# Kernel tuning notes

Hardware: AMD Instinct MI355X
Metric: run time of the kernel (lower is better)

Reference implementation:

```python
import jax, jax.numpy as jnp
import numpy as np

B, N, D = 8, 192, 768   # batch of docs, events per doc, embed_dim
H = 150                 # Score hidden_dim
PAD = -1000.0           # pad_and_stack fill value


def setup_inputs() -> dict:
    key = jax.random.key(0)
    ks = jax.random.split(key, 7)
    s1 = 1.0 / np.sqrt(3 * D)
    s2 = 1.0 / np.sqrt(H)
    return {
        "event_embed": jax.random.normal(ks[0], (B, N, D), jnp.float32),
        "W1": jax.random.normal(ks[1], (3 * D, H), jnp.float32) * s1,
        "b1": jnp.zeros((H,), jnp.float32),
        "W2": jax.random.normal(ks[2], (H, H), jnp.float32) * s2,
        "b2": jnp.zeros((H,), jnp.float32),
        "W3": jax.random.normal(ks[3], (H, 1), jnp.float32) * s2,
        "b3": jnp.zeros((1,), jnp.float32),
    }


def reference(event_embed, W1, b1, W2, b2, W3, b3):
    Bq, Nq, Dq = event_embed.shape
    # antecedent pairs: for each event i, all k < i (row-major, matches torch loop order)
    rows, cols = jnp.tril_indices(Nq, k=-1)          # [P], P = N*(N-1)/2
    i_g = event_embed[:, rows]                        # [B, P, D]
    j_g = event_embed[:, cols]                        # [B, P, D]
    pairs = jnp.concatenate([i_g, j_g, i_g * j_g], axis=-1)  # [B, P, 3D]
    # Score MLP (dropout is identity at inference)
    h = jax.nn.relu(pairs @ W1 + b1)                  # [B, P, H]
    h = jax.nn.relu(h @ W2 + b2)                      # [B, P, H]
    s = (h @ W3 + b3)[..., 0]                         # [B, P]
    # Scatter pair scores into [B, N, N]; diagonal stays 0 = epsilon score.
    logits = jnp.zeros((Bq, Nq, Nq), event_embed.dtype).at[:, rows, cols].set(s)
    tri = jnp.tril(jnp.ones((Nq, Nq), dtype=bool))    # valid cols: k <= i (incl epsilon)
    masked = jnp.where(tri, logits, -jnp.inf)
    probs = jax.nn.softmax(masked, axis=-1)           # ragged softmax per event row
    return jnp.where(tri, probs, jnp.asarray(PAD, probs.dtype))  # pad_and_stack(value=-1000)
```

## Files before the change

### kernel.cpp

```cpp
#include <hip/hip_runtime.h>
#include <hip/hip_bf16.h>

#define NSEQ   192
#define PADV   -1000.0f
#define NEGINF -1.0e30f

typedef __bf16 bf16x8 __attribute__((ext_vector_type(8)));
typedef float  f32x4  __attribute__((ext_vector_type(4)));

__device__ __forceinline__ void glds16(const void* g, void* l) {
  __builtin_amdgcn_global_load_lds(
      (const __attribute__((address_space(1))) unsigned int*)g,
      (__attribute__((address_space(3))) unsigned int*)l, 16, 0, 0);
}

#define MFMA16(a, b, c) __builtin_amdgcn_mfma_f32_16x16x32_bf16((a), (b), (c), 0, 0, 0)

__global__ __launch_bounds__(256) void prep_pack(const float* __restrict__ W1,
                                                 const float* __restrict__ W2,
                                                 __bf16* __restrict__ W1abp,
                                                 __bf16* __restrict__ W1cp,
                                                 __bf16* __restrict__ W2p) {
  int idx = blockIdx.x * 256 + threadIdx.x;
  if (idx < 245760) {
    int e = idx & 7, l = (idx >> 3) & 63, t = idx >> 9;
    int ct = t % 20, kk = t / 20;
    int k = kk * 32 + ((l >> 4) << 3) + e;
    int hp = ct * 16 + (l & 15);
    int col = (hp < 160) ? hp : hp - 160;
    int rbase = (hp < 160) ? 0 : 768;
    float v = (col < 150) ? W1[(size_t)(rbase + k) * 150 + col] : 0.f;
    W1abp[idx] = (__bf16)v;
  } else if (idx < 393216) {
    int j = idx - 245760;
    int kk = j / 6144, rem = j % 6144;
    int q = rem >> 9, l = (rem >> 3) & 63, e = rem & 7;
    int k = kk * 32 + ((l >> 4) << 3) + e;
    int h = q * 16 + (l & 15);
    float v = (q < 10 && h < 150) ? W1[(size_t)(1536 + k) * 150 + h] : 0.f;
    W1cp[j] = (__bf16)v;
  } else {
    int j = idx - 393216;
    int s = j / 6144, rem = j % 6144;
    int q = rem >> 9, l = (rem >> 3) & 63, e = rem & 7;
    int k = s * 32 + ((l >> 4) << 3) + e;
    int h = q * 16 + (l & 15);
    float v = (q < 10 && k < 150 && h < 150) ? W2[(size_t)k * 150 + h] : 0.f;
    W2p[j] = (__bf16)v;
  }
}

__global__ __launch_bounds__(256) void prep_gemm(const float* __restrict__ E,
                                                 const __bf16* __restrict__ W1abp,
                                                 float* __restrict__ A12) {
  int tid = threadIdx.x;
  int w = tid >> 6, l = tid & 63, m = l & 15, kg = l >> 4;
  int mt = blockIdx.x >> 3;
  int c  = blockIdx.x & 7;
  const float* ep = E + (size_t)(mt * 16 + m) * 768 + c * 96;

  f32x4 acc[5];
#pragma unroll
  for (int u = 0; u < 5; ++u) acc[u] = (f32x4){0.f, 0.f, 0.f, 0.f};

#pragma unroll
  for (int kk = 0; kk < 3; ++kk) {
    int k = kk * 32 + kg * 8;
    f32x4 x0 = *(const f32x4*)(ep + k);
    f32x4 x1 = *(const f32x4*)(ep + k + 4);
    bf16x8 af;
#pragma unroll
    for (int e = 0; e < 4; ++e) { af[e] = (__bf16)x0[e]; af[e + 4] = (__bf16)x1[e]; }
    const bf16x8* wp = (const bf16x8*)W1abp + (size_t)(((c * 3 + kk) * 20) + w * 5) * 64 + l;
#pragma unroll
    for (int u = 0; u < 5; ++u)
      acc[u] = MFMA16(af, wp[u * 64], acc[u]);
  }
#pragma unroll
  for (int u = 0; u < 5; ++u)
#pragma unroll
    for (int r = 0; r < 4; ++r)
      atomicAdd(&A12[(size_t)(mt * 16 + kg * 4 + r) * 320 + (w * 5 + u) * 16 + m], acc[u][r]);
}

__global__ __launch_bounds__(256, 2) void pair_mlp(
    const float* __restrict__ E, const float* __restrict__ A12,
    const __bf16* __restrict__ W1cp, const __bf16* __restrict__ W2p,
    const float* __restrict__ b1, const float* __restrict__ b2,
    const float* __restrict__ W3, const float* __restrict__ b3,
    float* __restrict__ out) {
  __shared__ alignas(16) char pool[73728];
  __bf16* Wb  = (__bf16*)pool;
  char*   eib = pool + 24576;
  char*   ejb = pool + 49152;
  char*   h1b = pool + 24576;

  const int tid = threadIdx.x;
  const int w = tid >> 6, l = tid & 63;
  const int m = l & 15, kg = l >> 4;

  int bid = blockIdx.x;
  int blk = (bid & 7) * 78 + (bid >> 3);
  int b = blk / 78, r0 = blk - b * 78;
  int it = (int)((sqrtf(8.f * (float)r0 + 1.f) - 1.f) * 0.5f);
  while (it * (it + 1) / 2 > r0) --it;
  while ((it + 1) * (it + 2) / 2 <= r0) ++it;
  int jt = r0 - it * (it + 1) / 2;

  const int ibase = b * NSEQ + it * 16;
  const int jbase = b * NSEQ + jt * 16;

#pragma unroll
  for (int q = 0; q < 3; ++q)
    glds16(W1cp + (size_t)(w * 3 + q) * 512 + l * 8, Wb + (w * 3 + q) * 512);

  {
    int r = tid >> 4, c0 = tid & 15;
    const float* si = E + (size_t)(ibase + r) * 768;
    const float* sj = E + (size_t)(jbase + r) * 768;
#pragma unroll
    for (int p = 0; p < 6; ++p) {
      int c = c0 + 16 * p;
      int cs = c ^ (r & 7);
      f32x4 a0 = *(const f32x4*)(si + cs * 8);
      f32x4 a1 = *(const f32x4*)(si + cs * 8 + 4);
      f32x4 b0 = *(const f32x4*)(sj + cs * 8);
      f32x4 b1q = *(const f32x4*)(sj + cs * 8 + 4);
      bf16x8 vi, vj;
#pragma unroll
      for (int e = 0; e < 4; ++e) {
        vi[e] = (__bf16)a0[e]; vi[e + 4] = (__bf16)a1[e];
        vj[e] = (__bf16)b0[e]; vj[e + 4] = (__bf16)b1q[e];
      }
      *(bf16x8*)(eib + r * 1536 + c * 16) = vi;
      *(bf16x8*)(ejb + r * 1536 + c * 16) = vj;
    }
  }

  f32x4 acc1[10][4];
#pragma unroll
  for (int ct = 0; ct < 10; ++ct) {
    f32x4 a1v = *(const f32x4*)(A12 + (size_t)(ibase + m) * 320 + ct * 16 + kg * 4);
    f32x4 b1v;
#pragma unroll
    for (int r = 0; r < 4; ++r) {
      int h = ct * 16 + kg * 4 + r;
      b1v[r] = (h < 150) ? b1[h] : 0.f;
    }
#pragma unroll
    for (int pt = 0; pt < 4; ++pt) {
      f32x4 a2v = *(const f32x4*)(A12 + (size_t)(jbase + w * 4 + pt) * 320 + 160 + ct * 16 + kg * 4);
#pragma unroll
      for (int r = 0; r < 4; ++r) acc1[ct][pt][r] = a1v[r] + a2v[r] + b1v[r];
    }
  }

  __syncthreads();

  for (int kk = 0; kk < 24; ++kk) {
    if (kk < 23) {
#pragma unroll
      for (int q = 0; q < 3; ++q)
        glds16(W1cp + ((size_t)(kk + 1) * 12 + w * 3 + q) * 512 + l * 8,
               Wb + (((kk + 1) & 1) * 12 + w * 3 + q) * 512);
      asm volatile("s_waitcnt vmcnt(3)" ::: "memory");
    } else {
      asm volatile("s_waitcnt vmcnt(0)" ::: "memory");
    }
    __builtin_amdgcn_s_barrier();

    const __bf16* wbuf = Wb + (kk & 1) * 6144;
    int cbase = kk * 4 + kg;
    bf16x8 eiv = *(const bf16x8*)(eib + m * 1536 + (cbase ^ (m & 7)) * 16);
    float eif[8];
#pragma unroll
    for (int e = 0; e < 8; ++e) eif[e] = (float)eiv[e];
    bf16x8 pf[4];
#pragma unroll
    for (int pt = 0; pt < 4; ++pt) {
      int jr = w * 4 + pt;
      bf16x8 ejv = *(const bf16x8*)(ejb + jr * 1536 + (cbase ^ (jr & 7)) * 16);
#pragma unroll
      for (int e = 0; e < 8; ++e)
        pf[pt][e] = (__bf16)(eif[e] * (float)ejv[e]);
    }
    __builtin_amdgcn_s_setprio(1);
#pragma unroll
    for (int ct = 0; ct < 10; ++ct) {
      bf16x8 wf = *(const bf16x8*)(wbuf + ct * 512 + l * 8);
#pragma unroll
      for (int pt = 0; pt < 4; ++pt)
        acc1[ct][pt] = MFMA16(wf, pf[pt], acc1[ct][pt]);
    }
    __builtin_amdgcn_s_setprio(0);
    __builtin_amdgcn_s_barrier();
  }

  auto write_h1 = [&](int ptL, int pt) {
    char* hb = h1b + w * 10752 + ptL * 5376 + m * 336;
#pragma unroll
    for (int ct = 0; ct < 10; ++ct) {
      union { __bf16 h[4]; unsigned u[2]; } cv;
      cv.h[0] = (__bf16)fmaxf(acc1[ct][pt][0], 0.f);
      cv.h[1] = (__bf16)fmaxf(acc1[ct][pt][1], 0.f);
      cv.h[2] = (__bf16)fmaxf(acc1[ct][pt][2], 0.f);
      cv.h[3] = (__bf16)fmaxf(acc1[ct][pt][3], 0.f);
      *(unsigned*)(hb + ct * 32 + kg * 8)     = cv.u[0];
      *(unsigned*)(hb + ct * 32 + kg * 8 + 4) = cv.u[1];
    }
  };
  write_h1(0, 0);
  write_h1(1, 1);

  float w3v[10], b2v[10];
#pragma unroll
  for (int ct = 0; ct < 10; ++ct) {
    int h = ct * 16 + m;
    w3v[ct] = (h < 150) ? W3[h] : 0.f;
    b2v[ct] = (h < 150) ? b2[h] : 0.f;
  }
  float b3v = b3[0];

#pragma unroll
  for (int q = 0; q < 3; ++q)
    glds16(W2p + (size_t)(w * 3 + q) * 512 + l * 8, Wb + (w * 3 + q) * 512);

  f32x4 acc2[10][2];
#pragma unroll
  for (int ct = 0; ct < 10; ++ct) {
    acc2[ct][0] = (f32x4){0.f, 0.f, 0.f, 0.f};
    acc2[ct][1] = (f32x4){0.f, 0.f, 0.f, 0.f};
  }

  for (int skk = 0; skk < 10; ++skk) {
    int s = (skk >= 5) ? skk - 5 : skk;
    if (skk == 5) { write_h1(0, 2); write_h1(1, 3); }
    if (skk < 9) {
      int n = skk + 1;
      int sl = (n >= 5) ? n - 5 : n;
#pragma unroll
      for (int q = 0; q < 3; ++q)
        glds16(W2p + ((size_t)sl * 12 + w * 3 + q) * 512 + l * 8,
               Wb + ((n & 1) * 12 + w * 3 + q) * 512);
      asm volatile("s_waitcnt vmcnt(3)" ::: "memory");
    } else {
      asm volatile("s_waitcnt vmcnt(0)" ::: "memory");
    }
    __builtin_amdgcn_s_barrier();

    const __bf16* wbuf = Wb + (skk & 1) * 6144;
    bf16x8 af0 = *(const bf16x8*)(h1b + w * 10752 +        m * 336 + s * 64 + kg * 16);
    bf16x8 af1 = *(const bf16x8*)(h1b + w * 10752 + 5376 + m * 336 + s * 64 + kg * 16);
    __builtin_amdgcn_s_setprio(1);
#pragma unroll
    for (int ct = 0; ct < 10; ++ct) {
      bf16x8 wf = *(const bf16x8*)(wbuf + ct * 512 + l * 8);
      acc2[ct][0] = MFMA16(af0, wf, acc2[ct][0]);
      acc2[ct][1] = MFMA16(af1, wf, acc2[ct][1]);
    }
    __builtin_amdgcn_s_setprio(0);

    if (s == 4) {
      int pass = skk / 5;
#pragma unroll
      for (int ptL = 0; ptL < 2; ++ptL) {
        float part[4] = {0.f, 0.f, 0.f, 0.f};
#pragma unroll
        for (int ct = 0; ct < 10; ++ct)
#pragma unroll
          for (int r = 0; r < 4; ++r)
            part[r] += fmaxf(acc2[ct][ptL][r] + b2v[ct], 0.f) * w3v[ct];
#pragma unroll
        for (int off = 8; off >= 1; off >>= 1)
#pragma unroll
          for (int r = 0; r < 4; ++r) part[r] += __shfl_xor(part[r], off, 16);
        int jl = jt * 16 + w * 4 + pass * 2 + ptL;
#pragma unroll
        for (int r = 0; r < 4; ++r) {
          if (m == r) {
            int il = it * 16 + kg * 4 + r;
            if (jl < il)
              out[(size_t)(b * NSEQ + il) * NSEQ + jl] = part[r] + b3v;
          }
        }
#pragma unroll
        for (int ct = 0; ct < 10; ++ct)
          acc2[ct][ptL] = (f32x4){0.f, 0.f, 0.f, 0.f};
      }
    }
    __builtin_amdgcn_s_barrier();
  }
}

__global__ __launch_bounds__(256) void softmax_rows(float* __restrict__ out) {
  int w = threadIdx.x >> 6, l = threadIdx.x & 63;
  int blk = blockIdx.x * 4 + w;
  int i = blk % NSEQ;
  size_t base = (size_t)blk * NSEQ;
  float v[3];
  float mx = NEGINF;
#pragma unroll
  for (int t = 0; t < 3; ++t) {
    int j = l + 64 * t;
    float x = (j < i) ? out[base + j] : (j == i ? 0.f : NEGINF);
    v[t] = x;
    mx = fmaxf(mx, x);
  }
#pragma unroll
  for (int off = 32; off >= 1; off >>= 1) mx = fmaxf(mx, __shfl_xor(mx, off, 64));
  float s = 0.f;
#pragma unroll
  for (int t = 0; t < 3; ++t) s += __expf(v[t] - mx);
#pragma unroll
  for (int off = 32; off >= 1; off >>= 1) s += __shfl_xor(s, off, 64);
  float inv = 1.0f / s;
#pragma unroll
  for (int t = 0; t < 3; ++t) {
    int j = l + 64 * t;
    out[base + j] = (j <= i) ? __expf(v[t] - mx) * inv : PADV;
  }
}

extern "C" void kernel_launch(void* const* d_in, const int* in_sizes, int n_in,
                              void* d_out, int out_size, void* d_ws, size_t ws_size,
                              hipStream_t stream) {
  const float* E  = (const float*)d_in[0];
  const float* W1 = (const float*)d_in[1];
  const float* b1 = (const float*)d_in[2];
  const float* W2 = (const float*)d_in[3];
  const float* b2 = (const float*)d_in[4];
  const float* W3 = (const float*)d_in[5];
  const float* b3 = (const float*)d_in[6];
  float* out = (float*)d_out;

  char* ws = (char*)d_ws;
  float*  A12   = (float*)(ws);
  __bf16* W1abp = (__bf16*)(ws + 1966080);
  __bf16* W1cp  = (__bf16*)(ws + 2457600);
  __bf16* W2p   = (__bf16*)(ws + 2752512);

  hipMemsetAsync(A12, 0, 1966080, stream);
  prep_pack<<<1656, 256, 0, stream>>>(W1, W2, W1abp, W1cp, W2p);
  prep_gemm<<<768, 256, 0, stream>>>(E, W1abp, A12);
  pair_mlp<<<624, 256, 0, stream>>>(E, A12, W1cp, W2p, b1, b2, W3, b3, out);
  softmax_rows<<<384, 256, 0, stream>>>(out);
}
```

Before: 100.4 us.

## Use 8 waves per pair_mlp block with fewer accumulators per wave

pair_mlp now launches 512 threads instead of 256. Each wave handles 2 j-rows instead of 4, which halves the acc1/acc2 register tiles and targets higher occupancy (launch bounds 512,4). Weight-tile loads are split across the first 6 waves. The h1 buffer is re-laid-out with an XOR swizzle, and the second GEMM swaps operand order so the final W3 reduction needs only two cross-lane shuffles. b1 is pre-padded in prep_pack, and b2/W3 are staged in shared memory. The cost is less MFMA reuse of each loaded weight fragment per wave and more barrier participants.

```diff
diff --git a/kernel.cpp b/kernel.cpp
--- a/kernel.cpp
+++ b/kernel.cpp
@@ -18,9 +18,11 @@
 
 __global__ __launch_bounds__(256) void prep_pack(const float* __restrict__ W1,
                                                  const float* __restrict__ W2,
+                                                 const float* __restrict__ b1,
                                                  __bf16* __restrict__ W1abp,
                                                  __bf16* __restrict__ W1cp,
-                                                 __bf16* __restrict__ W2p) {
+                                                 __bf16* __restrict__ W2p,
+                                                 float* __restrict__ b1p) {
   int idx = blockIdx.x * 256 + threadIdx.x;
   if (idx < 245760) {
     int e = idx & 7, l = (idx >> 3) & 63, t = idx >> 9;
@@ -39,7 +41,7 @@
     int h = q * 16 + (l & 15);
     float v = (q < 10 && h < 150) ? W1[(size_t)(1536 + k) * 150 + h] : 0.f;
     W1cp[j] = (__bf16)v;
-  } else {
+  } else if (idx < 423936) {
     int j = idx - 393216;
     int s = j / 6144, rem = j % 6144;
     int q = rem >> 9, l = (rem >> 3) & 63, e = rem & 7;
@@ -47,6 +49,9 @@
     int h = q * 16 + (l & 15);
     float v = (q < 10 && k < 150 && h < 150) ? W2[(size_t)k * 150 + h] : 0.f;
     W2p[j] = (__bf16)v;
+  } else if (idx < 424096) {
+    int h = idx - 423936;
+    b1p[h] = (h < 150) ? b1[h] : 0.f;
   }
 }
 
@@ -83,21 +88,20 @@
       atomicAdd(&A12[(size_t)(mt * 16 + kg * 4 + r) * 320 + (w * 5 + u) * 16 + m], acc[u][r]);
 }
 
-__global__ __launch_bounds__(256, 2) void pair_mlp(
+__global__ __launch_bounds__(512, 4) void pair_mlp(
     const float* __restrict__ E, const float* __restrict__ A12,
     const __bf16* __restrict__ W1cp, const __bf16* __restrict__ W2p,
-    const float* __restrict__ b1, const float* __restrict__ b2,
+    const float* __restrict__ b1p, const float* __restrict__ b2,
     const float* __restrict__ W3, const float* __restrict__ b3,
     float* __restrict__ out) {
-  __shared__ alignas(16) char pool[73728];
-  __bf16* Wb  = (__bf16*)pool;
-  char*   eib = pool + 24576;
-  char*   ejb = pool + 49152;
-  char*   h1b = pool + 24576;
+  __shared__ alignas(16) char pool[75648];
+  char* eib = pool + 24576;
+  char* ejb = pool + 49152;
 
   const int tid = threadIdx.x;
   const int w = tid >> 6, l = tid & 63;
   const int m = l & 15, kg = l >> 4;
+  const int jr0 = 2 * w, jr1 = 2 * w + 1;
 
   int bid = blockIdx.x;
   int blk = (bid & 7) * 78 + (bid >> 3);
@@ -110,183 +114,170 @@
   const int ibase = b * NSEQ + it * 16;
   const int jbase = b * NSEQ + jt * 16;
 
-#pragma unroll
-  for (int q = 0; q < 3; ++q)
-    glds16(W1cp + (size_t)(w * 3 + q) * 512 + l * 8, Wb + (w * 3 + q) * 512);
-
-  {
-    int r = tid >> 4, c0 = tid & 15;
-    const float* si = E + (size_t)(ibase + r) * 768;
-    const float* sj = E + (size_t)(jbase + r) * 768;
-#pragma unroll
-    for (int p = 0; p < 6; ++p) {
-      int c = c0 + 16 * p;
-      int cs = c ^ (r & 7);
-      f32x4 a0 = *(const f32x4*)(si + cs * 8);
-      f32x4 a1 = *(const f32x4*)(si + cs * 8 + 4);
-      f32x4 b0 = *(const f32x4*)(sj + cs * 8);
-      f32x4 b1q = *(const f32x4*)(sj + cs * 8 + 4);
-      bf16x8 vi, vj;
-#pragma unroll
-      for (int e = 0; e < 4; ++e) {
-        vi[e] = (__bf16)a0[e]; vi[e + 4] = (__bf16)a1[e];
-        vj[e] = (__bf16)b0[e]; vj[e + 4] = (__bf16)b1q[e];
-      }
-      *(bf16x8*)(eib + r * 1536 + c * 16) = vi;
-      *(bf16x8*)(ejb + r * 1536 + c * 16) = vj;
-    }
-  }
-
-  f32x4 acc1[10][4];
+  if (w < 6) {
+#pragma unroll
+    for (int q = 0; q < 2; ++q)
+      glds16(W1cp + (size_t)(2 * w + q) * 512 + l * 8,
+             pool + (2 * w + q) * 1024 + l * 16);
+  }
+
+#pragma unroll
+  for (int q = 0; q < 3; ++q) {
+    int t = tid + 512 * q;
+    int r = t / 96, d = t - (t / 96) * 96;
+    int sc = d ^ (r & 7);
+    const float* si = E + (size_t)(ibase + r) * 768 + sc * 8;
+    const float* sj = E + (size_t)(jbase + r) * 768 + sc * 8;
+    f32x4 a0 = *(const f32x4*)(si);
+    f32x4 a1 = *(const f32x4*)(si + 4);
+    f32x4 c0 = *(const f32x4*)(sj);
+    f32x4 c1 = *(const f32x4*)(sj + 4);
+    bf16x8 vi, vj;
+#pragma unroll
+    for (int e = 0; e < 4; ++e) {
+      vi[e] = (__bf16)a0[e]; vi[e + 4] = (__bf16)a1[e];
+      vj[e] = (__bf16)c0[e]; vj[e + 4] = (__bf16)c1[e];
+    }
+    *(bf16x8*)(eib + r * 1536 + d * 16) = vi;
+    *(bf16x8*)(ejb + r * 1536 + d * 16) = vj;
+  }
+
+  if (tid < 160) {
+    float* bwf = (float*)(pool + 73728);
+    bwf[tid]       = (tid < 150) ? b2[tid] : 0.f;
+    bwf[160 + tid] = (tid < 150) ? W3[tid] : 0.f;
+  }
+  float b3v = b3[0];
+
+  f32x4 acc1[10][2];
 #pragma unroll
   for (int ct = 0; ct < 10; ++ct) {
     f32x4 a1v = *(const f32x4*)(A12 + (size_t)(ibase + m) * 320 + ct * 16 + kg * 4);
-    f32x4 b1v;
-#pragma unroll
-    for (int r = 0; r < 4; ++r) {
-      int h = ct * 16 + kg * 4 + r;
-      b1v[r] = (h < 150) ? b1[h] : 0.f;
-    }
-#pragma unroll
-    for (int pt = 0; pt < 4; ++pt) {
-      f32x4 a2v = *(const f32x4*)(A12 + (size_t)(jbase + w * 4 + pt) * 320 + 160 + ct * 16 + kg * 4);
-#pragma unroll
-      for (int r = 0; r < 4; ++r) acc1[ct][pt][r] = a1v[r] + a2v[r] + b1v[r];
+    f32x4 b1v = *(const f32x4*)(b1p + ct * 16 + kg * 4);
+#pragma unroll
+    for (int pt = 0; pt < 2; ++pt) {
+      f32x4 a2v = *(const f32x4*)(A12 + (size_t)(jbase + jr0 + pt) * 320 + 160 + ct * 16 + kg * 4);
+      acc1[ct][pt] = a1v + a2v + b1v;
     }
   }
 
   __syncthreads();
 
-  for (int kk = 0; kk < 24; ++kk) {
-    if (kk < 23) {
-#pragma unroll
-      for (int q = 0; q < 3; ++q)
-        glds16(W1cp + ((size_t)(kk + 1) * 12 + w * 3 + q) * 512 + l * 8,
-               Wb + (((kk + 1) & 1) * 12 + w * 3 + q) * 512);
-      asm volatile("s_waitcnt vmcnt(3)" ::: "memory");
-    } else {
-      asm volatile("s_waitcnt vmcnt(0)" ::: "memory");
+  auto compute = [&](int kk) {
+    const __bf16* wb = (const __bf16*)(pool + (kk & 1) * 12288);
+    int cb = kk * 4 + kg;
+    bf16x8 eiv = *(const bf16x8*)(eib + m * 1536 + ((cb ^ (m & 7)) << 4));
+    bf16x8 ej0 = *(const bf16x8*)(ejb + jr0 * 1536 + ((cb ^ (jr0 & 7)) << 4));
+    bf16x8 ej1 = *(const bf16x8*)(ejb + jr1 * 1536 + ((cb ^ (jr1 & 7)) << 4));
+    bf16x8 pf0, pf1;
+#pragma unroll
+    for (int e = 0; e < 8; ++e) {
+      float ei = (float)eiv[e];
+      pf0[e] = (__bf16)(ei * (float)ej0[e]);
+      pf1[e] = (__bf16)(ei * (float)ej1[e]);
+    }
+    __builtin_amdgcn_s_setprio(1);
+#pragma unroll
+    for (int ct = 0; ct < 10; ++ct) {
+      bf16x8 wf = *(const bf16x8*)(wb + ct * 512 + l * 8);
+      acc1[ct][0] = MFMA16(wf, pf0, acc1[ct][0]);
+      acc1[ct][1] = MFMA16(wf, pf1, acc1[ct][1]);
+    }
+    __builtin_amdgcn_s_setprio(0);
+  };
+
+  for (int kk = 0; kk < 23; ++kk) {
+    if (w < 6) {
+#pragma unroll
+      for (int q = 0; q < 2; ++q)
+        glds16(W1cp + ((size_t)(kk + 1) * 12 + 2 * w + q) * 512 + l * 8,
+               pool + ((kk + 1) & 1) * 12288 + (2 * w + q) * 1024 + l * 16);
+      asm volatile("s_waitcnt vmcnt(2)" ::: "memory");
     }
     __builtin_amdgcn_s_barrier();
-
-    const __bf16* wbuf = Wb + (kk & 1) * 6144;
-    int cbase = kk * 4 + kg;
-    bf16x8 eiv = *(const bf16x8*)(eib + m * 1536 + (cbase ^ (m & 7)) * 16);
-    float eif[8];
-#pragma unroll
-    for (int e = 0; e < 8; ++e) eif[e] = (float)eiv[e];
-    bf16x8 pf[4];
-#pragma unroll
-    for (int pt = 0; pt < 4; ++pt) {
-      int jr = w * 4 + pt;
-      bf16x8 ejv = *(const bf16x8*)(ejb + jr * 1536 + (cbase ^ (jr & 7)) * 16);
-#pragma unroll
-      for (int e = 0; e < 8; ++e)
-        pf[pt][e] = (__bf16)(eif[e] * (float)ejv[e]);
-    }
-    __builtin_amdgcn_s_setprio(1);
-#pragma unroll
-    for (int ct = 0; ct < 10; ++ct) {
-      bf16x8 wf = *(const bf16x8*)(wbuf + ct * 512 + l * 8);
-#pragma unroll
-      for (int pt = 0; pt < 4; ++pt)
-        acc1[ct][pt] = MFMA16(wf, pf[pt], acc1[ct][pt]);
-    }
-    __builtin_amdgcn_s_setprio(0);
+    compute(kk);
     __builtin_amdgcn_s_barrier();
   }
-
-  auto write_h1 = [&](int ptL, int pt) {
-    char* hb = h1b + w * 10752 + ptL * 5376 + m * 336;
+  if (w < 6) asm volatile("s_waitcnt vmcnt(0)" ::: "memory");
+  __builtin_amdgcn_s_barrier();
+  compute(23);
+  __builtin_amdgcn_s_barrier();
+
+  char* hb = pool + 24576 + w * 6144;
+  auto write_h1 = [&](int p) {
 #pragma unroll
     for (int ct = 0; ct < 10; ++ct) {
       union { __bf16 h[4]; unsigned u[2]; } cv;
-      cv.h[0] = (__bf16)fmaxf(acc1[ct][pt][0], 0.f);
-      cv.h[1] = (__bf16)fmaxf(acc1[ct][pt][1], 0.f);
-      cv.h[2] = (__bf16)fmaxf(acc1[ct][pt][2], 0.f);
-      cv.h[3] = (__bf16)fmaxf(acc1[ct][pt][3], 0.f);
-      *(unsigned*)(hb + ct * 32 + kg * 8)     = cv.u[0];
-      *(unsigned*)(hb + ct * 32 + kg * 8 + 4) = cv.u[1];
+      cv.h[0] = (__bf16)fmaxf(acc1[ct][p][0], 0.f);
+      cv.h[1] = (__bf16)fmaxf(acc1[ct][p][1], 0.f);
+      cv.h[2] = (__bf16)fmaxf(acc1[ct][p][2], 0.f);
+      cv.h[3] = (__bf16)fmaxf(acc1[ct][p][3], 0.f);
+      int c = (2 * ct + (kg >> 1)) ^ (m & 7);
+      char* dst = hb + m * 384 + c * 16 + (kg & 1) * 8;
+      *(unsigned*)(dst)     = cv.u[0];
+      *(unsigned*)(dst + 4) = cv.u[1];
     }
   };
-  write_h1(0, 0);
-  write_h1(1, 1);
-
-  float w3v[10], b2v[10];
-#pragma unroll
-  for (int ct = 0; ct < 10; ++ct) {
-    int h = ct * 16 + m;
-    w3v[ct] = (h < 150) ? W3[h] : 0.f;
-    b2v[ct] = (h < 150) ? b2[h] : 0.f;
-  }
-  float b3v = b3[0];
-
-#pragma unroll
-  for (int q = 0; q < 3; ++q)
-    glds16(W2p + (size_t)(w * 3 + q) * 512 + l * 8, Wb + (w * 3 + q) * 512);
-
-  f32x4 acc2[10][2];
-#pragma unroll
-  for (int ct = 0; ct < 10; ++ct) {
-    acc2[ct][0] = (f32x4){0.f, 0.f, 0.f, 0.f};
-    acc2[ct][1] = (f32x4){0.f, 0.f, 0.f, 0.f};
-  }
-
-  for (int skk = 0; skk < 10; ++skk) {
-    int s = (skk >= 5) ? skk - 5 : skk;
-    if (skk == 5) { write_h1(0, 2); write_h1(1, 3); }
-    if (skk < 9) {
-      int n = skk + 1;
-      int sl = (n >= 5) ? n - 5 : n;
-#pragma unroll
-      for (int q = 0; q < 3; ++q)
-        glds16(W2p + ((size_t)sl * 12 + w * 3 + q) * 512 + l * 8,
-               Wb + ((n & 1) * 12 + w * 3 + q) * 512);
-      asm volatile("s_waitcnt vmcnt(3)" ::: "memory");
+  write_h1(0);
+  if (w < 6) {
+#pragma unroll
+    for (int q = 0; q < 2; ++q)
+      glds16(W2p + (size_t)(2 * w + q) * 512 + l * 8,
+             pool + (2 * w + q) * 1024 + l * 16);
+  }
+
+  const float* bwp = (const float*)(pool + 73728);
+  f32x4 acc2[10];
+#pragma unroll
+  for (int ct = 0; ct < 10; ++ct) acc2[ct] = (f32x4){0.f, 0.f, 0.f, 0.f};
+
+  for (int rr = 0; rr < 10; ++rr) {
+    int p = rr / 5, s = rr - p * 5;
+    if (rr == 5) write_h1(1);
+    if (rr < 9) {
+      int ns = (rr + 1 >= 5) ? rr + 1 - 5 : rr + 1;
+      if (w < 6) {
+#pragma unroll
+        for (int q = 0; q < 2; ++q)
+          glds16(W2p + ((size_t)ns * 12 + 2 * w + q) * 512 + l * 8,
+                 pool + ((rr + 1) & 1) * 12288 + (2 * w + q) * 1024 + l * 16);
+        asm volatile("s_waitcnt vmcnt(2)" ::: "memory");
+      }
     } else {
-      asm volatile("s_waitcnt vmcnt(0)" ::: "memory");
+      if (w < 6) asm volatile("s_waitcnt vmcnt(0)" ::: "memory");
     }
     __builtin_amdgcn_s_barrier();
 
-    const __bf16* wbuf = Wb + (skk & 1) * 6144;
-    bf16x8 af0 = *(const bf16x8*)(h1b + w * 10752 +        m * 336 + s * 64 + kg * 16);
-    bf16x8 af1 = *(const bf16x8*)(h1b + w * 10752 + 5376 + m * 336 + s * 64 + kg * 16);
+    const __bf16* wb2 = (const __bf16*)(pool + (rr & 1) * 12288);
+    bf16x8 af = *(const bf16x8*)(hb + m * 384 + (((4 * s + kg) ^ (m & 7)) << 4));
     __builtin_amdgcn_s_setprio(1);
 #pragma unroll
     for (int ct = 0; ct < 10; ++ct) {
-      bf16x8 wf = *(const bf16x8*)(wbuf + ct * 512 + l * 8);
-      acc2[ct][0] = MFMA16(af0, wf, acc2[ct][0]);
-      acc2[ct][1] = MFMA16(af1, wf, acc2[ct][1]);
+      bf16x8 wf = *(const bf16x8*)(wb2 + ct * 512 + l * 8);
+      acc2[ct] = MFMA16(wf, af, acc2[ct]);
     }
     __builtin_amdgcn_s_setprio(0);
 
     if (s == 4) {
-      int pass = skk / 5;
-#pragma unroll
-      for (int ptL = 0; ptL < 2; ++ptL) {
-        float part[4] = {0.f, 0.f, 0.f, 0.f};
-#pragma unroll
-        for (int ct = 0; ct < 10; ++ct)
-#pragma unroll
-          for (int r = 0; r < 4; ++r)
-            part[r] += fmaxf(acc2[ct][ptL][r] + b2v[ct], 0.f) * w3v[ct];
-#pragma unroll
-        for (int off = 8; off >= 1; off >>= 1)
-#pragma unroll
-          for (int r = 0; r < 4; ++r) part[r] += __shfl_xor(part[r], off, 16);
-        int jl = jt * 16 + w * 4 + pass * 2 + ptL;
-#pragma unroll
-        for (int r = 0; r < 4; ++r) {
-          if (m == r) {
-            int il = it * 16 + kg * 4 + r;
-            if (jl < il)
-              out[(size_t)(b * NSEQ + il) * NSEQ + jl] = part[r] + b3v;
-          }
-        }
-#pragma unroll
-        for (int ct = 0; ct < 10; ++ct)
-          acc2[ct][ptL] = (f32x4){0.f, 0.f, 0.f, 0.f};
+      float sum = 0.f;
+#pragma unroll
+      for (int ct = 0; ct < 10; ++ct) {
+        f32x4 b2q = *(const f32x4*)(bwp + ct * 16 + kg * 4);
+        f32x4 w3q = *(const f32x4*)(bwp + 160 + ct * 16 + kg * 4);
+#pragma unroll
+        for (int r = 0; r < 4; ++r)
+          sum += fmaxf(acc2[ct][r] + b2q[r], 0.f) * w3q[r];
       }
+      sum += __shfl_xor(sum, 16, 64);
+      sum += __shfl_xor(sum, 32, 64);
+      if (kg == 0) {
+        int il = it * 16 + m;
+        int jl = jt * 16 + 2 * w + p;
+        if (jl < il)
+          out[(size_t)(b * NSEQ + il) * NSEQ + jl] = sum + b3v;
+      }
+#pragma unroll
+      for (int ct = 0; ct < 10; ++ct) acc2[ct] = (f32x4){0.f, 0.f, 0.f, 0.f};
     }
     __builtin_amdgcn_s_barrier();
   }
@@ -338,10 +329,11 @@
   __bf16* W1abp = (__bf16*)(ws + 1966080);
   __bf16* W1cp  = (__bf16*)(ws + 2457600);
   __bf16* W2p   = (__bf16*)(ws + 2752512);
+  float*  b1p   = (float*)(ws + 2813952);
 
   hipMemsetAsync(A12, 0, 1966080, stream);
-  prep_pack<<<1656, 256, 0, stream>>>(W1, W2, W1abp, W1cp, W2p);
+  prep_pack<<<1657, 256, 0, stream>>>(W1, W2, b1, W1abp, W1cp, W2p, b1p);
   prep_gemm<<<768, 256, 0, stream>>>(E, W1abp, A12);
-  pair_mlp<<<624, 256, 0, stream>>>(E, A12, W1cp, W2p, b1, b2, W3, b3, out);
+  pair_mlp<<<624, 512, 0, stream>>>(E, A12, W1cp, W2p, b1p, b2, W3, b3, out);
   softmax_rows<<<384, 256, 0, stream>>>(out);
 }
```

After: 100.3 us. About the same (-0.1%).
